# Kernel optimization log

Hardware: AMD Instinct MI355X
Metric: run time of the kernel (lower is better)

## Reference

```python
import jax, jax.numpy as jnp
import numpy as np

N_NODES = 50000
N_EDGES = 1600000
IN_CH = 128
HID_CH = 128


def setup_inputs() -> dict:
    key = jax.random.key(0)
    ks = jax.random.split(key, 8)
    node_embed = jax.random.normal(ks[0], (N_NODES, IN_CH), dtype=jnp.float32)
    node_pos = jax.random.normal(ks[1], (N_NODES, 3), dtype=jnp.float32)
    edge_index = jax.random.randint(ks[2], (2, N_EDGES), 0, N_NODES, dtype=jnp.int64)
    # Linear weights stored as [in, out] so y = x @ W + b (matches torch x @ W.T + b)
    W_res = jax.random.normal(ks[3], (IN_CH, HID_CH), dtype=jnp.float32) / np.sqrt(IN_CH)
    W_msg = jax.random.normal(ks[4], (2 * IN_CH + 1, HID_CH), dtype=jnp.float32) / np.sqrt(2 * IN_CH + 1)
    b_msg = jax.random.normal(ks[5], (HID_CH,), dtype=jnp.float32) * 0.01
    W_upd = jax.random.normal(ks[6], (IN_CH + HID_CH, HID_CH), dtype=jnp.float32) / np.sqrt(IN_CH + HID_CH)
    b_upd = jax.random.normal(ks[7], (HID_CH,), dtype=jnp.float32) * 0.01
    return {"node_embed": node_embed, "node_pos": node_pos, "edge_index": edge_index,
            "W_res": W_res, "W_msg": W_msg, "b_msg": b_msg, "W_upd": W_upd, "b_upd": b_upd}


def reference(node_embed, node_pos, edge_index, W_res, W_msg, b_msg, W_upd, b_upd):
    row, col = edge_index[0], edge_index[1]
    # squared distance per edge: [E, 1]
    diff = node_pos[row] - node_pos[col]
    dist = jnp.sum(diff * diff, axis=1, keepdims=True)
    # message MLP on concat(src, tgt, dist): [E, 2*in+1] -> [E, hidden]
    msg_in = jnp.concatenate([node_embed[row], node_embed[col], dist], axis=-1)
    msg = jax.nn.relu(msg_in @ W_msg + b_msg)
    # scatter-sum messages into target nodes (index = col, as in original)
    aggr = jax.ops.segment_sum(msg, col, num_segments=N_NODES)
    upd_in = jnp.concatenate([node_embed, aggr], axis=-1)
    new_node_embed = node_embed @ W_res + jax.nn.relu(upd_in @ W_upd + b_upd)
    return new_node_embed
```

## Files before the change

kernel.cpp:

```cpp
#include <hip/hip_runtime.h>
#include <hip/hip_bf16.h>
#include <cstdint>


typedef __bf16 bf16x8 __attribute__((ext_vector_type(8)));
typedef float floatx4 __attribute__((ext_vector_type(4)));
typedef float floatx2 __attribute__((ext_vector_type(2)));
typedef unsigned int uintx4 __attribute__((ext_vector_type(4)));

#define BUCKET_CAP 128
#define NBINS 256
#define BIN_CAP 10240
#define PASS2_SPLIT 4

__device__ __forceinline__ ushort f2bf(float f) {
  union { float f; uint i; } v; v.f = f;
  uint r = v.i + 0x7fff + ((v.i >> 16) & 1);
  return (ushort)(r >> 16);
}
__device__ __forceinline__ bf16x8 load_frag(const ushort* p) {
  uint4 v = *(const uint4*)p;
  return __builtin_bit_cast(bf16x8, v);
}
__device__ __forceinline__ floatx2 pmax0(floatx2 a) {
#if __has_builtin(__builtin_elementwise_max)
  return __builtin_elementwise_max(a, (floatx2)(0.f));
#else
  floatx2 r; r.x = fmaxf(a.x, 0.f); r.y = fmaxf(a.y, 0.f); return r;
#endif
}
__device__ __forceinline__ floatx2 cvtpk2(uint qu) {
#if __has_builtin(__builtin_amdgcn_cvt_pk_f32_fp8)
  return __builtin_amdgcn_cvt_pk_f32_fp8((int)qu, false);
#else
  floatx2 o = {__builtin_amdgcn_cvt_f32_fp8((int)qu, 0),
               __builtin_amdgcn_cvt_f32_fp8((int)qu, 1)};
  return o;
#endif
}

struct WSrc { const float* s[5]; };

__global__ __launch_bounds__(256) void k01_cast_bin(
    const float* __restrict__ embed, ushort* __restrict__ Eb, int n4, int nb_cast,
    WSrc ws, ushort* __restrict__ Wt,
    const int* __restrict__ ei, int E, const float* __restrict__ pos,
    uint* __restrict__ bin_cursor, uint2* __restrict__ binned, int bb)
{
  __shared__ uint hist[NBINS];
  __shared__ uint sbase[NBINS];
  __shared__ uint lcur[NBINS];

  if ((int)blockIdx.x >= bb) {
    int cb = blockIdx.x - bb;
    if (cb < nb_cast) {
      int i = cb * 256 + threadIdx.x;
      if (i < n4) {
        float4 v = ((const float4*)embed)[i];
        ushort4 o;
        o.x = f2bf(v.x); o.y = f2bf(v.y); o.z = f2bf(v.z); o.w = f2bf(v.w);
        ((ushort4*)Eb)[i] = o;
      }
      return;
    }
    int wb = cb - nb_cast;
    const float* s = ws.s[wb];
    ushort* d = Wt + wb * 16384;
    for (int i = threadIdx.x; i < 16384; i += 256) {
      int k = i >> 7, n = i & 127;
      d[n * 128 + k] = f2bf(s[i]);
    }
    return;
  }

  const int t = threadIdx.x;
  hist[t] = 0;
  __syncthreads();

  const int e0 = blockIdx.x * 2048 + t * 8;
  int rr[8], cc[8];
  uint2 rec[8];
  bool any = (e0 < E);
  if (any) {
    int4 r0 = ((const int4*)(ei + e0))[0];
    int4 r1 = ((const int4*)(ei + e0))[1];
    int4 c0 = ((const int4*)(ei + E + e0))[0];
    int4 c1 = ((const int4*)(ei + E + e0))[1];
    rr[0]=r0.x; rr[1]=r0.y; rr[2]=r0.z; rr[3]=r0.w;
    rr[4]=r1.x; rr[5]=r1.y; rr[6]=r1.z; rr[7]=r1.w;
    cc[0]=c0.x; cc[1]=c0.y; cc[2]=c0.z; cc[3]=c0.w;
    cc[4]=c1.x; cc[5]=c1.y; cc[6]=c1.z; cc[7]=c1.w;
#pragma unroll
    for (int j = 0; j < 8; ++j) {
      bool val = (e0 + j < E);
      int r = val ? rr[j] : 0, c = val ? cc[j] : 0;
      float dx = pos[3 * r + 0] - pos[3 * c + 0];
      float dy = pos[3 * r + 1] - pos[3 * c + 1];
      float dz = pos[3 * r + 2] - pos[3 * c + 2];
      float dist = dx * dx + dy * dy + dz * dz;
      rec[j].x = ((uint)c << 16) | (uint)r;
      rec[j].y = (uint)f2bf(dist);
      if (val) atomicAdd(&hist[c >> 8], 1u);
    }
  }
  __syncthreads();
  uint h = hist[t];
  sbase[t] = h ? atomicAdd(bin_cursor + t, h) : 0u;
  lcur[t] = 0;
  __syncthreads();
  if (any) {
#pragma unroll
    for (int j = 0; j < 8; ++j) {
      if (e0 + j < E) {
        int b = cc[j] >> 8;
        uint ofs = atomicAdd(&lcur[b], 1u);
        uint idx = sbase[b] + ofs;
        if (idx < BIN_CAP)
          binned[(size_t)b * BIN_CAP + idx] = rec[j];
      }
    }
  }
}

__global__ __launch_bounds__(256) void k2_proj_pass2(
    const ushort* __restrict__ Ab, int M, int rt,
    const ushort* __restrict__ W1t, const ushort* __restrict__ W2t,
    const float* __restrict__ b_msg,
    unsigned char* __restrict__ P1, ushort* __restrict__ P2b,
    const uint* __restrict__ bin_cursor, const uint2* __restrict__ binned,
    int* __restrict__ counts, uint* __restrict__ recs)
{
  if ((int)blockIdx.x >= rt) {
    int b = blockIdx.x - rt;
    int bin = b / PASS2_SPLIT, part = b % PASS2_SPLIT;
    int cnt = (int)min(bin_cursor[bin], (uint)BIN_CAP);
    int s0 = (int)((long)cnt * part / PASS2_SPLIT);
    int s1 = (int)((long)cnt * (part + 1) / PASS2_SPLIT);
    const uint2* src = binned + (size_t)bin * BIN_CAP;
    for (int i = s0 + threadIdx.x; i < s1; i += 256) {
      uint2 rec = src[i];
      uint c = rec.x >> 16;
      int slot = atomicAdd(counts + c, 1);
      if (slot < BUCKET_CAP)
        recs[(size_t)c * BUCKET_CAP + slot] = (rec.x << 16) | (rec.y & 0xffffu);
    }
    return;
  }

  const int wv = threadIdx.x >> 6, lane = threadIdx.x & 63;
  const int q = lane >> 4, lr = lane & 15;
  const int m0 = blockIdx.x * 32;
  const int n0 = wv * 32;

  const ushort* Wt2[2] = {W1t, W2t};
  bf16x8 bfr[2][2][4];
#pragma unroll
  for (int ws = 0; ws < 2; ++ws)
#pragma unroll
    for (int nt = 0; nt < 2; ++nt) {
      int colc = n0 + nt * 16 + lr;
#pragma unroll
      for (int kc = 0; kc < 4; ++kc)
        bfr[ws][nt][kc] = load_frag(Wt2[ws] + colc * 128 + kc * 32 + q * 8);
    }

  floatx4 z = {0.f, 0.f, 0.f, 0.f};
  floatx4 acc[2][2][2];
#pragma unroll
  for (int ws = 0; ws < 2; ++ws)
#pragma unroll
    for (int mt = 0; mt < 2; ++mt)
#pragma unroll
      for (int nt = 0; nt < 2; ++nt) acc[ws][mt][nt] = z;

  const int r0 = min(m0 + lr, M - 1);
  const int r1 = min(m0 + 16 + lr, M - 1);
#pragma unroll
  for (int kc = 0; kc < 4; ++kc) {
    bf16x8 a0 = load_frag(Ab + (size_t)r0 * 128 + kc * 32 + q * 8);
    bf16x8 a1 = load_frag(Ab + (size_t)r1 * 128 + kc * 32 + q * 8);
#pragma unroll
    for (int ws = 0; ws < 2; ++ws)
#pragma unroll
      for (int nt = 0; nt < 2; ++nt) {
        acc[ws][0][nt] = __builtin_amdgcn_mfma_f32_16x16x32_bf16(a0, bfr[ws][nt][kc], acc[ws][0][nt], 0, 0, 0);
        acc[ws][1][nt] = __builtin_amdgcn_mfma_f32_16x16x32_bf16(a1, bfr[ws][nt][kc], acc[ws][1][nt], 0, 0, 0);
      }
  }

#pragma unroll
  for (int nt = 0; nt < 2; ++nt) {
    int colc = n0 + nt * 16 + lr;
    float bias = b_msg[colc];
#pragma unroll
    for (int mt = 0; mt < 2; ++mt)
#pragma unroll
      for (int i = 0; i < 4; ++i) {
        int r = m0 + mt * 16 + q * 4 + i;
        if (r < M) {
          int p8 = __builtin_amdgcn_cvt_pk_fp8_f32(acc[0][mt][nt][i], 0.f, 0, false);
          P1[(size_t)r * 128 + colc] = (unsigned char)(p8 & 0xff);
          P2b[(size_t)r * 128 + colc] = f2bf(acc[1][mt][nt][i] + bias);
        }
      }
  }
}

__global__ __launch_bounds__(256) void aggregate(const int* __restrict__ counts,
                                                 const uint* __restrict__ recs,
                                                 const unsigned char* __restrict__ P1,
                                                 const ushort* __restrict__ P2b,
                                                 const float* __restrict__ wd,
                                                 ushort* __restrict__ aggr, int M)
{
  const int lane = threadIdx.x & 63;
  const int ch = lane * 2;
  const int wid = blockIdx.x * 4 + (threadIdx.x >> 6);
  const int nw = gridDim.x * 4;

  float2 wl = *(const float2*)(wd + ch);
  floatx2 wv = {wl.x, wl.y};

  for (int n = wid; n < M; n += nw) {
    uint p2u = *(const uint*)(P2b + (size_t)n * 128 + ch);
    floatx2 p2 = {__int_as_float((int)(p2u << 16)),
                  __int_as_float((int)(p2u & 0xffff0000u))};

    const int cnt = min(counts[n], BUCKET_CAP);
    const uint* base = recs + (size_t)n * BUCKET_CAP;

    floatx2 accA = {0.f, 0.f}, accB = {0.f, 0.f};

    auto edge = [&](uint rec, floatx2& acc) {
      float d = __int_as_float((int)(rec << 16));
      uint off = ((rec >> 9) & 0x007fff80u) | (uint)ch;
      uint qu = (uint)*(const ushort*)(P1 + off);
#if __has_builtin(__builtin_elementwise_fma)
      floatx2 u = __builtin_elementwise_fma((floatx2)(d), wv, p2);
#else
      floatx2 u = (floatx2)(d) * wv + p2;
#endif
      floatx2 t = cvtpk2(qu) + u;
      acc += pmax0(t);
    };

    int i = 0;
    for (; i + 8 <= cnt; i += 8) {
      uintx4 ra = __builtin_nontemporal_load((const uintx4*)(base + i));
      uintx4 rb = __builtin_nontemporal_load((const uintx4*)(base + i + 4));
      edge(ra.x, accA); edge(ra.y, accB); edge(ra.z, accA); edge(ra.w, accB);
      edge(rb.x, accA); edge(rb.y, accB); edge(rb.z, accA); edge(rb.w, accB);
    }
    for (; i < cnt; ++i) edge(base[i], accA);

    floatx2 acc = accA + accB;
    uint o = (uint)f2bf(acc.x) | ((uint)f2bf(acc.y) << 16);
    *(uint*)(aggr + (size_t)n * 128 + ch) = o;
  }
}

__global__ __launch_bounds__(256) void gemm_upd_mfma(
    const ushort* __restrict__ Eb, const ushort* __restrict__ Gb, int M,
    const ushort* __restrict__ Wu1t, const ushort* __restrict__ Wu2t,
    const ushort* __restrict__ Wrt, const float* __restrict__ b_upd,
    float* __restrict__ out)
{
  const int wv = threadIdx.x >> 6, lane = threadIdx.x & 63;
  const int q = lane >> 4, lr = lane & 15;
  const int m0 = blockIdx.x * 32;
  const int n0 = wv * 32;

  bf16x8 b1[2][4], b2[2][4], br[2][4];
#pragma unroll
  for (int nt = 0; nt < 2; ++nt) {
    int colc = n0 + nt * 16 + lr;
#pragma unroll
    for (int kc = 0; kc < 4; ++kc) {
      b1[nt][kc] = load_frag(Wu1t + colc * 128 + kc * 32 + q * 8);
      b2[nt][kc] = load_frag(Wu2t + colc * 128 + kc * 32 + q * 8);
      br[nt][kc] = load_frag(Wrt  + colc * 128 + kc * 32 + q * 8);
    }
  }

  floatx4 z = {0.f, 0.f, 0.f, 0.f};
  floatx4 acc_u[2][2], acc_r[2][2];
#pragma unroll
  for (int mt = 0; mt < 2; ++mt)
#pragma unroll
    for (int nt = 0; nt < 2; ++nt) { acc_u[mt][nt] = z; acc_r[mt][nt] = z; }

  const int r0 = min(m0 + lr, M - 1);
  const int r1 = min(m0 + 16 + lr, M - 1);
#pragma unroll
  for (int kc = 0; kc < 4; ++kc) {
    bf16x8 ae0 = load_frag(Eb + (size_t)r0 * 128 + kc * 32 + q * 8);
    bf16x8 ae1 = load_frag(Eb + (size_t)r1 * 128 + kc * 32 + q * 8);
    bf16x8 ag0 = load_frag(Gb + (size_t)r0 * 128 + kc * 32 + q * 8);
    bf16x8 ag1 = load_frag(Gb + (size_t)r1 * 128 + kc * 32 + q * 8);
#pragma unroll
    for (int nt = 0; nt < 2; ++nt) {
      acc_u[0][nt] = __builtin_amdgcn_mfma_f32_16x16x32_bf16(ae0, b1[nt][kc], acc_u[0][nt], 0, 0, 0);
      acc_u[1][nt] = __builtin_amdgcn_mfma_f32_16x16x32_bf16(ae1, b1[nt][kc], acc_u[1][nt], 0, 0, 0);
      acc_u[0][nt] = __builtin_amdgcn_mfma_f32_16x16x32_bf16(ag0, b2[nt][kc], acc_u[0][nt], 0, 0, 0);
      acc_u[1][nt] = __builtin_amdgcn_mfma_f32_16x16x32_bf16(ag1, b2[nt][kc], acc_u[1][nt], 0, 0, 0);
      acc_r[0][nt] = __builtin_amdgcn_mfma_f32_16x16x32_bf16(ae0, br[nt][kc], acc_r[0][nt], 0, 0, 0);
      acc_r[1][nt] = __builtin_amdgcn_mfma_f32_16x16x32_bf16(ae1, br[nt][kc], acc_r[1][nt], 0, 0, 0);
    }
  }

#pragma unroll
  for (int nt = 0; nt < 2; ++nt) {
    int colc = n0 + nt * 16 + lr;
    float bias = b_upd[colc];
#pragma unroll
    for (int mt = 0; mt < 2; ++mt)
#pragma unroll
      for (int i = 0; i < 4; ++i) {
        int r = m0 + mt * 16 + q * 4 + i;
        if (r < M)
          out[(size_t)r * 128 + colc] = acc_r[mt][nt][i] + fmaxf(acc_u[mt][nt][i] + bias, 0.f);
      }
  }
}

extern "C" void kernel_launch(void* const* d_in, const int* in_sizes, int n_in,
                              void* d_out, int out_size, void* d_ws, size_t ws_size,
                              hipStream_t stream)
{
  const float* embed = (const float*)d_in[0];
  const float* pos   = (const float*)d_in[1];
  const int*   ei    = (const int*)d_in[2];
  const float* W_res = (const float*)d_in[3];
  const float* W_msg = (const float*)d_in[4];
  const float* b_msg = (const float*)d_in[5];
  const float* W_upd = (const float*)d_in[6];
  const float* b_upd = (const float*)d_in[7];
  float* out = (float*)d_out;

  const int M = in_sizes[0] / 128;
  const int E = in_sizes[2] / 2;

  ushort* Eb = (ushort*)d_ws;
  unsigned char* P1f8 = (unsigned char*)(Eb + (size_t)M * 128);
  ushort* P2b = (ushort*)(P1f8 + (size_t)M * 128);
  ushort* Gb  = P2b + (size_t)M * 128;
  ushort* Wt  = Gb  + (size_t)M * 128;
  uint*   recs = (uint*)(Wt + 5 * 16384);
  uint2*  binned = (uint2*)(recs + (size_t)M * BUCKET_CAP);
  int*    counts = (int*)(binned + (size_t)NBINS * BIN_CAP);
  uint*   bin_cursor = (uint*)(counts + M);

  (void)hipMemsetAsync(counts, 0, (size_t)(M + NBINS) * sizeof(int), stream);

  WSrc wsrc;
  wsrc.s[0] = W_msg;
  wsrc.s[1] = W_msg + 128 * 128;
  wsrc.s[2] = W_res;
  wsrc.s[3] = W_upd;
  wsrc.s[4] = W_upd + 128 * 128;

  int n4 = M * 128 / 4;
  int nb_cast = (n4 + 255) / 256;
  int bb = (E + 2047) / 2048;
  k01_cast_bin<<<bb + nb_cast + 5, 256, 0, stream>>>(
      embed, Eb, n4, nb_cast, wsrc, Wt, ei, E, pos, bin_cursor, binned, bb);

  int rt = (M + 31) / 32;
  k2_proj_pass2<<<rt + NBINS * PASS2_SPLIT, 256, 0, stream>>>(
      Eb, M, rt, Wt, Wt + 16384, b_msg, P1f8, P2b,
      bin_cursor, binned, counts, recs);

  int ab = min((M + 3) / 4, 2048);
  aggregate<<<ab, 256, 0, stream>>>(counts, recs, P1f8, P2b,
                                    W_msg + 256 * 128, Gb, M);

  gemm_upd_mfma<<<rt, 256, 0, stream>>>(Eb, Gb, M, Wt + 3 * 16384, Wt + 4 * 16384,
                                        Wt + 2 * 16384, b_upd, out);
}
```

Baseline: 277.7 us.

## Move distance computation to pass2, shrink binned records, pad bin cursors

The squared-distance computation moves from the binning kernel into the pass2 scatter, so binned records drop from 8 bytes to 4 bytes (packed col/row only). This halves the write and read traffic of the intermediate bin buffer and removes the position gathers from the first kernel. Pass2 now gathers positions itself, with a 4-way unrolled loop to overlap the loads. Global bin cursors are also spaced 32 entries apart so their atomics do not contend on shared cache lines, at the cost of a slightly larger memset.

```diff
diff --git a/kernel.cpp b/kernel.cpp
--- a/kernel.cpp
+++ b/kernel.cpp
@@ -12,6 +12,7 @@
 #define NBINS 256
 #define BIN_CAP 10240
 #define PASS2_SPLIT 4
+#define CUR_STRIDE 32
 
 __device__ __forceinline__ ushort f2bf(float f) {
   union { float f; uint i; } v; v.f = f;
@@ -44,8 +45,8 @@
 __global__ __launch_bounds__(256) void k01_cast_bin(
     const float* __restrict__ embed, ushort* __restrict__ Eb, int n4, int nb_cast,
     WSrc ws, ushort* __restrict__ Wt,
-    const int* __restrict__ ei, int E, const float* __restrict__ pos,
-    uint* __restrict__ bin_cursor, uint2* __restrict__ binned, int bb)
+    const int* __restrict__ ei, int E,
+    uint* __restrict__ bin_cursor, uint* __restrict__ binned, int bb)
 {
   __shared__ uint hist[NBINS];
   __shared__ uint sbase[NBINS];
@@ -79,7 +80,6 @@
 
   const int e0 = blockIdx.x * 2048 + t * 8;
   int rr[8], cc[8];
-  uint2 rec[8];
   bool any = (e0 < E);
   if (any) {
     int4 r0 = ((const int4*)(ei + e0))[0];
@@ -92,20 +92,12 @@
     cc[4]=c1.x; cc[5]=c1.y; cc[6]=c1.z; cc[7]=c1.w;
 #pragma unroll
     for (int j = 0; j < 8; ++j) {
-      bool val = (e0 + j < E);
-      int r = val ? rr[j] : 0, c = val ? cc[j] : 0;
-      float dx = pos[3 * r + 0] - pos[3 * c + 0];
-      float dy = pos[3 * r + 1] - pos[3 * c + 1];
-      float dz = pos[3 * r + 2] - pos[3 * c + 2];
-      float dist = dx * dx + dy * dy + dz * dz;
-      rec[j].x = ((uint)c << 16) | (uint)r;
-      rec[j].y = (uint)f2bf(dist);
-      if (val) atomicAdd(&hist[c >> 8], 1u);
+      if (e0 + j < E) atomicAdd(&hist[cc[j] >> 8], 1u);
     }
   }
   __syncthreads();
   uint h = hist[t];
-  sbase[t] = h ? atomicAdd(bin_cursor + t, h) : 0u;
+  sbase[t] = h ? atomicAdd(bin_cursor + t * CUR_STRIDE, h) : 0u;
   lcur[t] = 0;
   __syncthreads();
   if (any) {
@@ -116,7 +108,7 @@
         uint ofs = atomicAdd(&lcur[b], 1u);
         uint idx = sbase[b] + ofs;
         if (idx < BIN_CAP)
-          binned[(size_t)b * BIN_CAP + idx] = rec[j];
+          binned[(size_t)b * BIN_CAP + idx] = ((uint)cc[j] << 16) | (uint)rr[j];
       }
     }
   }
@@ -125,24 +117,50 @@
 __global__ __launch_bounds__(256) void k2_proj_pass2(
     const ushort* __restrict__ Ab, int M, int rt,
     const ushort* __restrict__ W1t, const ushort* __restrict__ W2t,
-    const float* __restrict__ b_msg,
+    const float* __restrict__ b_msg, const float* __restrict__ pos,
     unsigned char* __restrict__ P1, ushort* __restrict__ P2b,
-    const uint* __restrict__ bin_cursor, const uint2* __restrict__ binned,
+    const uint* __restrict__ bin_cursor, const uint* __restrict__ binned,
     int* __restrict__ counts, uint* __restrict__ recs)
 {
   if ((int)blockIdx.x >= rt) {
     int b = blockIdx.x - rt;
     int bin = b / PASS2_SPLIT, part = b % PASS2_SPLIT;
-    int cnt = (int)min(bin_cursor[bin], (uint)BIN_CAP);
+    int cnt = (int)min(bin_cursor[bin * CUR_STRIDE], (uint)BIN_CAP);
     int s0 = (int)((long)cnt * part / PASS2_SPLIT);
     int s1 = (int)((long)cnt * (part + 1) / PASS2_SPLIT);
-    const uint2* src = binned + (size_t)bin * BIN_CAP;
-    for (int i = s0 + threadIdx.x; i < s1; i += 256) {
-      uint2 rec = src[i];
-      uint c = rec.x >> 16;
+    const uint* src = binned + (size_t)bin * BIN_CAP;
+
+    int i = s0 + threadIdx.x;
+    for (; i + 768 < s1; i += 1024) {
+      uint rc[4];
+      rc[0] = src[i]; rc[1] = src[i + 256]; rc[2] = src[i + 512]; rc[3] = src[i + 768];
+      float d[4];
+#pragma unroll
+      for (int j = 0; j < 4; ++j) {
+        uint r = rc[j] & 0xffffu, c = rc[j] >> 16;
+        float dx = pos[3 * r + 0] - pos[3 * c + 0];
+        float dy = pos[3 * r + 1] - pos[3 * c + 1];
+        float dz = pos[3 * r + 2] - pos[3 * c + 2];
+        d[j] = dx * dx + dy * dy + dz * dz;
+      }
+#pragma unroll
+      for (int j = 0; j < 4; ++j) {
+        uint c = rc[j] >> 16;
+        int slot = atomicAdd(counts + c, 1);
+        if (slot < BUCKET_CAP)
+          recs[(size_t)c * BUCKET_CAP + slot] = (rc[j] << 16) | (uint)f2bf(d[j]);
+      }
+    }
+    for (; i < s1; i += 256) {
+      uint rc = src[i];
+      uint r = rc & 0xffffu, c = rc >> 16;
+      float dx = pos[3 * r + 0] - pos[3 * c + 0];
+      float dy = pos[3 * r + 1] - pos[3 * c + 1];
+      float dz = pos[3 * r + 2] - pos[3 * c + 2];
+      float dist = dx * dx + dy * dy + dz * dz;
       int slot = atomicAdd(counts + c, 1);
       if (slot < BUCKET_CAP)
-        recs[(size_t)c * BUCKET_CAP + slot] = (rec.x << 16) | (rec.y & 0xffffu);
+        recs[(size_t)c * BUCKET_CAP + slot] = (rc << 16) | (uint)f2bf(dist);
     }
     return;
   }
@@ -346,11 +364,11 @@
   ushort* Gb  = P2b + (size_t)M * 128;
   ushort* Wt  = Gb  + (size_t)M * 128;
   uint*   recs = (uint*)(Wt + 5 * 16384);
-  uint2*  binned = (uint2*)(recs + (size_t)M * BUCKET_CAP);
+  uint*   binned = (uint*)(recs + (size_t)M * BUCKET_CAP);
   int*    counts = (int*)(binned + (size_t)NBINS * BIN_CAP);
   uint*   bin_cursor = (uint*)(counts + M);
 
-  (void)hipMemsetAsync(counts, 0, (size_t)(M + NBINS) * sizeof(int), stream);
+  (void)hipMemsetAsync(counts, 0, (size_t)(M + NBINS * CUR_STRIDE) * sizeof(int), stream);
 
   WSrc wsrc;
   wsrc.s[0] = W_msg;
@@ -363,11 +381,11 @@
   int nb_cast = (n4 + 255) / 256;
   int bb = (E + 2047) / 2048;
   k01_cast_bin<<<bb + nb_cast + 5, 256, 0, stream>>>(
-      embed, Eb, n4, nb_cast, wsrc, Wt, ei, E, pos, bin_cursor, binned, bb);
+      embed, Eb, n4, nb_cast, wsrc, Wt, ei, E, bin_cursor, binned, bb);
 
   int rt = (M + 31) / 32;
   k2_proj_pass2<<<rt + NBINS * PASS2_SPLIT, 256, 0, stream>>>(
-      Eb, M, rt, Wt, Wt + 16384, b_msg, P1f8, P2b,
+      Eb, M, rt, Wt, Wt + 16384, b_msg, pos, P1f8, P2b,
       bin_cursor, binned, counts, recs);
 
   int ab = min((M + 3) / 4, 2048);
```

Result: no change. 276.8 us (-0.3%).
